# Optimization experiments

Hardware: AMD Instinct MI355X
Metric: run time of the kernel (lower is better)

Reference implementation:

```python
import jax, jax.numpy as jnp
import numpy as np

TEMPERATURE = 0.07
MSE_WEIGHT = 0.5
SUPCON_WEIGHT = 1.0
EPS = 1e-12  # F.normalize default eps

P_POS = 4000
P_NEG = 4000
NVOX = 32768
FEAT = 128


def setup_inputs() -> dict:
    key = jax.random.key(0)
    k1, k2, k3, k4, k5 = jax.random.split(key, 5)
    Zs = jax.random.normal(k1, (1, FEAT, NVOX), dtype=jnp.float32)
    pos_idx = jax.random.randint(k2, (P_POS,), 0, NVOX, dtype=jnp.int32)
    neg_idx = jax.random.randint(k3, (P_NEG,), 0, NVOX, dtype=jnp.int32)
    feature_diff = jax.random.normal(k4, (1, FEAT, 32, 32, 32), dtype=jnp.float32)
    input_diff = jax.random.normal(k5, (1, FEAT, 32, 32, 32), dtype=jnp.float32)
    return {"Zs": Zs, "pos_idx": pos_idx, "neg_idx": neg_idx,
            "feature_diff": feature_diff, "input_diff": input_diff}


def _l2_normalize_rows(x):
    # F.normalize(x, dim=1): x / max(||x||_2, eps)
    n = jnp.sqrt(jnp.sum(x * x, axis=1, keepdims=True))
    return x / jnp.maximum(n, EPS)


def _supcon_loss(Zs, pos_idx, neg_idx):
    feats = Zs[0].T                                   # [Nvox, F]
    pixels = jnp.concatenate([feats[pos_idx], feats[neg_idx]], axis=0)  # [N, F]
    n = pixels.shape[0]
    labels = jnp.concatenate([jnp.ones((P_POS,), jnp.int32),
                              jnp.zeros((P_NEG,), jnp.int32)])
    pixels = _l2_normalize_rows(pixels)
    dot = jnp.matmul(pixels, pixels.T) / TEMPERATURE  # [N, N]
    dot = _l2_normalize_rows(dot)                     # row-normalize the NxN matrix
    expm = jnp.exp(dot)
    class_mask = (labels[:, None] == labels[None, :]) & ~jnp.eye(n, dtype=bool)
    pos_term = expm * class_mask
    pos_term = jnp.where(pos_term == 0, 1.0, pos_term)
    denom = jnp.sum(expm * ~class_mask, axis=1) - jnp.diagonal(expm)  # [N]
    full_term = jnp.log(pos_term) - jnp.log(denom)[None, :]
    return -(1.0 / n) * jnp.sum(full_term)


def reference(Zs, pos_idx, neg_idx, feature_diff, input_diff):
    supcon = _supcon_loss(Zs, pos_idx, neg_idx)
    mse = jnp.mean((feature_diff - input_diff) ** 2)
    return SUPCON_WEIGHT * supcon + MSE_WEIGHT * mse
```

## Files before the change

### kernel.cpp

```cpp
#include <hip/hip_runtime.h>
#include <hip/hip_bf16.h>
#include <math.h>

typedef unsigned short u16;
typedef float  f32x4  __attribute__((ext_vector_type(4)));
typedef __bf16 bf16x8 __attribute__((ext_vector_type(8)));

#define NPOS   4000
#define LDP    136
#define TILE_CH 2176
#define MSE_N  4194304
#define GATHER_B 2000
#define MSE_B    512

__device__ __forceinline__ void load_lds16(const void* g, void* l) {
  __builtin_amdgcn_global_load_lds(
      (const __attribute__((address_space(1))) unsigned int*)g,
      (__attribute__((address_space(3))) unsigned int*)l, 16, 0, 0);
}

__device__ __forceinline__ float bf2f(u16 h) {
  unsigned u = ((unsigned)h) << 16;
  return __builtin_bit_cast(float, u);
}

struct Args {
  const float* Zs; const int* pos; const int* neg;
  const float4* fd; const float4* idf;
  u16* Pc; u16* Prow; float* G; float* S;
  float* qpos; float* qneg; float* sdpos; float* sdneg;
  float* msepart; float* out;
};

__global__ __launch_bounds__(256) void prep_k(Args a) {
  int blk = blockIdx.x, tid = threadIdx.x;
  int wave = tid >> 6, lane = tid & 63;
  if (blk < GATHER_B) {
    int row = blk * 4 + wave;
    int col = (row < NPOS) ? row : (4096 + row - NPOS);
    int v   = (row < NPOS) ? a.pos[row] : a.neg[row - NPOS];
    const float* zc = a.Zs + v;
    float x0 = zc[(size_t)lane << 15];
    float x1 = zc[(size_t)(lane + 64) << 15];
    float s = x0 * x0 + x1 * x1;
    #pragma unroll
    for (int o = 1; o < 64; o <<= 1) s += __shfl_xor(s, o, 64);
    float inv = 1.0f / fmaxf(sqrtf(s), 1e-12f);
    __hip_bfloat16 h0 = __float2bfloat16(x0 * inv);
    __hip_bfloat16 h1 = __float2bfloat16(x1 * inv);
    u16 b0 = *(u16*)&h0, b1 = *(u16*)&h1;
    a.Prow[(size_t)col * LDP + lane]      = b0;
    a.Prow[(size_t)col * LDP + lane + 64] = b1;
    size_t cbase = (size_t)(col >> 7) * (128 * LDP) + (col & 127);
    a.Pc[cbase + (size_t)lane * LDP]        = b0;
    a.Pc[cbase + (size_t)(lane + 64) * LDP] = b1;
  } else if (blk < GATHER_B + MSE_B) {
    int b = blk - GATHER_B;
    float ms = 0.f;
    for (int idx = b * 256 + tid; idx < MSE_N / 4; idx += MSE_B * 256) {
      float4 u = a.fd[idx], w = a.idf[idx];
      float dx = u.x - w.x, dy = u.y - w.y, dz = u.z - w.z, dv = u.w - w.w;
      ms += dx * dx + dy * dy + dz * dz + dv * dv;
    }
    #pragma unroll
    for (int o = 1; o < 64; o <<= 1) ms += __shfl_xor(ms, o, 64);
    __shared__ float red[4];
    if (lane == 0) red[wave] = ms;
    __syncthreads();
    if (tid == 0) a.msepart[b] = red[0] + red[1] + red[2] + red[3];
  } else {
    int ch = (blk == GATHER_B + MSE_B) ? 31 : 63;
    for (int e = tid; e < 128 * 96; e += 256) {
      int f = e / 96, c = 32 + e % 96;
      a.Pc[(size_t)ch * (128 * LDP) + (size_t)f * LDP + c] = 0;
    }
  }
}

__global__ __launch_bounds__(256) void syrk_k(Args a) {
  __shared__ __align__(16) u16 T0[128 * LDP];
  int blk = blockIdx.x, tid = threadIdx.x;
  int wave = tid >> 6, lane = tid & 63;
  int wm = (wave >> 1) << 6, wn = (wave & 1) << 6;
  int r = lane & 15, q = lane >> 4;
  int sf = tid >> 1, sh = tid & 1;
  float ssum = 0.f;
  f32x4 acc[4][4];
  #pragma unroll
  for (int x = 0; x < 4; ++x)
    #pragma unroll
    for (int y = 0; y < 4; ++y) {
      acc[x][y][0] = 0.f; acc[x][y][1] = 0.f; acc[x][y][2] = 0.f; acc[x][y][3] = 0.f;
    }
  for (int it = 0; it < 4; ++it) {
    const u16* g = a.Pc + (size_t)(blk * 4 + it) * (128 * LDP);
    #pragma unroll
    for (int k = 0; k < 9; ++k) {
      int cc = k * 256 + tid;
      if (cc < TILE_CH) load_lds16(g + cc * 8, &T0[cc * 8]);
    }
    __syncthreads();
    #pragma unroll
    for (int kk = 0; kk < 4; ++kk) {
      int k0 = kk * 32 + q * 8;
      bf16x8 af[4], bfr[4];
      #pragma unroll
      for (int t = 0; t < 4; ++t) {
        af[t]  = *(const bf16x8*)&T0[(wm + t * 16 + r) * LDP + k0];
        bfr[t] = *(const bf16x8*)&T0[(wn + t * 16 + r) * LDP + k0];
      }
      #pragma unroll
      for (int mt = 0; mt < 4; ++mt)
        #pragma unroll
        for (int nt = 0; nt < 4; ++nt)
          acc[mt][nt] = __builtin_amdgcn_mfma_f32_16x16x32_bf16(
              af[mt], bfr[nt], acc[mt][nt], 0, 0, 0);
    }
    {
      const u16* base = &T0[sf * LDP + sh * 64];
      #pragma unroll
      for (int vb = 0; vb < 8; ++vb) {
        bf16x8 v = *(const bf16x8*)&base[vb * 8];
        #pragma unroll
        for (int j = 0; j < 8; ++j) ssum += (float)v[j];
      }
    }
    __syncthreads();
  }
  float* Gf = a.G + (size_t)(blk >> 3) * 16384;
  #pragma unroll
  for (int mt = 0; mt < 4; ++mt)
    #pragma unroll
    for (int nt = 0; nt < 4; ++nt)
      #pragma unroll
      for (int reg = 0; reg < 4; ++reg) {
        int ar = wm + mt * 16 + q * 4 + reg;
        int bc = wn + nt * 16 + r;
        atomicAdd(&Gf[ar * 128 + bc], acc[mt][nt][reg]);
      }
  ssum += __shfl_xor(ssum, 1, 64);
  if (sh == 0) atomicAdd(&a.S[(blk >> 3) * 128 + sf], ssum);
}

__global__ __launch_bounds__(256) void quad_k(Args a) {
  __shared__ __align__(16) u16 T0[128 * LDP];
  __shared__ __align__(16) u16 T1[128 * LDP];
  __shared__ float Sl[256];
  __shared__ float qld[2][128];
  int cb = blockIdx.x & 63, set = blockIdx.x >> 6, tid = threadIdx.x;
  Sl[tid] = a.S[tid];
  const u16* gP = a.Prow + (size_t)cb * (128 * LDP);
  #pragma unroll
  for (int k = 0; k < 9; ++k) {
    int cc = k * 256 + tid;
    if (cc < TILE_CH) load_lds16(gP + cc * 8, &T1[cc * 8]);
  }
  {
    int f = tid >> 1, half = (tid & 1) * 64;
    const float4* gsrc = (const float4*)(a.G + (size_t)set * 16384 + f * 128 + half);
    #pragma unroll
    for (int j16 = 0; j16 < 16; ++j16) {
      float4 v = gsrc[j16];
      __hip_bfloat16 c0 = __float2bfloat16(v.x), c1 = __float2bfloat16(v.y);
      __hip_bfloat16 c2 = __float2bfloat16(v.z), c3 = __float2bfloat16(v.w);
      ushort4 pk = { *(u16*)&c0, *(u16*)&c1, *(u16*)&c2, *(u16*)&c3 };
      *(ushort4*)&T0[f * LDP + half + j16 * 4] = pk;
    }
  }
  __syncthreads();
  int wave = tid >> 6, lane = tid & 63;
  int wm = (wave >> 1) << 6, wn = (wave & 1) << 6;
  int r = lane & 15, q = lane >> 4;
  f32x4 acc[4][4];
  #pragma unroll
  for (int x = 0; x < 4; ++x)
    #pragma unroll
    for (int y = 0; y < 4; ++y) {
      acc[x][y][0] = 0.f; acc[x][y][1] = 0.f; acc[x][y][2] = 0.f; acc[x][y][3] = 0.f;
    }
  #pragma unroll
  for (int kk = 0; kk < 4; ++kk) {
    int k0 = kk * 32 + q * 8;
    bf16x8 af[4], bfr[4];
    #pragma unroll
    for (int t = 0; t < 4; ++t) {
      af[t]  = *(const bf16x8*)&T0[(wm + t * 16 + r) * LDP + k0];
      bfr[t] = *(const bf16x8*)&T1[(wn + t * 16 + r) * LDP + k0];
    }
    #pragma unroll
    for (int mt = 0; mt < 4; ++mt)
      #pragma unroll
      for (int nt = 0; nt < 4; ++nt)
        acc[mt][nt] = __builtin_amdgcn_mfma_f32_16x16x32_bf16(
            af[mt], bfr[nt], acc[mt][nt], 0, 0, 0);
  }
  float qv[4] = {0.f, 0.f, 0.f, 0.f};
  #pragma unroll
  for (int nt = 0; nt < 4; ++nt) {
    int il = wn + nt * 16 + r;
    #pragma unroll
    for (int mt = 0; mt < 4; ++mt) {
      const u16* pp = &T1[il * LDP + wm + mt * 16 + q * 4];
      #pragma unroll
      for (int reg = 0; reg < 4; ++reg)
        qv[nt] += acc[mt][nt][reg] * bf2f(pp[reg]);
    }
  }
  #pragma unroll
  for (int nt = 0; nt < 4; ++nt) {
    qv[nt] += __shfl_xor(qv[nt], 16, 64);
    qv[nt] += __shfl_xor(qv[nt], 32, 64);
  }
  int half = wm >> 6;
  if (q == 0) {
    #pragma unroll
    for (int nt = 0; nt < 4; ++nt) qld[half][wn + nt * 16 + r] = qv[nt];
  }
  __syncthreads();
  float* qarr = set ? a.qneg : a.qpos;
  if (tid < 128) qarr[cb * 128 + tid] = qld[0][tid] + qld[1][tid];
  if (set == 0) {
    int which = tid >> 7, sl = tid & 127;
    const float* Sv = &Sl[which * 128];
    float d = 0.f;
    #pragma unroll
    for (int fb = 0; fb < 16; ++fb) {
      const u16* pv = &T1[sl * LDP + fb * 8];
      #pragma unroll
      for (int j = 0; j < 8; ++j) d += Sv[fb * 8 + j] * bf2f(pv[j]);
    }
    (which ? a.sdneg : a.sdpos)[cb * 128 + sl] = d;
  }
}

__global__ __launch_bounds__(256) void final_k(Args a) {
  int tid = threadIdx.x;
  int wave = tid >> 6, lane = tid & 63;
  float lg = 0.f, sm = 0.f;
  for (int col = tid; col < 8192; col += 256) {
    bool isp = col < NPOS;
    bool isn = (col >= 4096) && (col < 4096 + NPOS);
    if (isp || isn) {
      float qp = a.qpos[col], qn = a.qneg[col];
      float c = 1.0f / sqrtf(qp + qn);
      float qo  = isp ? qn : qp;
      float sdo = isp ? a.sdneg[col] : a.sdpos[col];
      float sds = isp ? a.sdpos[col] : a.sdneg[col];
      float denom = 4000.0f + c * sdo + 0.5f * c * c * qo;
      lg += logf(denom);
      sm += c * (sds - 1.0f);
    }
  }
  float ms = a.msepart[tid] + a.msepart[tid + 256];
  #pragma unroll
  for (int o = 1; o < 64; o <<= 1) {
    lg += __shfl_xor(lg, o, 64);
    sm += __shfl_xor(sm, o, 64);
    ms += __shfl_xor(ms, o, 64);
  }
  __shared__ float redf[12];
  if (lane == 0) { redf[wave] = lg; redf[4 + wave] = sm; redf[8 + wave] = ms; }
  __syncthreads();
  if (tid == 0) {
    float lgs = redf[0] + redf[1] + redf[2] + redf[3];
    float sms = redf[4] + redf[5] + redf[6] + redf[7];
    float mss = redf[8] + redf[9] + redf[10] + redf[11];
    a.out[0] = lgs - sms * (1.0f / 8000.0f) + 0.5f * (mss * (1.0f / (float)MSE_N));
  }
}

extern "C" void kernel_launch(void* const* d_in, const int* in_sizes, int n_in,
                              void* d_out, int out_size, void* d_ws, size_t ws_size,
                              hipStream_t stream) {
  char* ws = (char*)d_ws;
  Args args;
  args.Zs  = (const float*)d_in[0];
  args.pos = (const int*)d_in[1];
  args.neg = (const int*)d_in[2];
  args.fd  = (const float4*)d_in[3];
  args.idf = (const float4*)d_in[4];
  args.out = (float*)d_out;

  args.Pc      = (u16*)(ws + 0);
  args.Prow    = (u16*)(ws + 2228224);
  args.G       = (float*)(ws + 4456448);
  args.S       = (float*)(ws + 4587520);
  args.qpos    = (float*)(ws + 4588544);
  args.qneg    = (float*)(ws + 4621312);
  args.sdpos   = (float*)(ws + 4654080);
  args.sdneg   = (float*)(ws + 4686848);
  args.msepart = (float*)(ws + 4719616);

  hipMemsetAsync(ws + 4456448, 0, 132096, stream);
  prep_k<<<GATHER_B + MSE_B + 2, 256, 0, stream>>>(args);
  syrk_k<<<16, 256, 0, stream>>>(args);
  quad_k<<<128, 256, 0, stream>>>(args);
  final_k<<<1, 256, 0, stream>>>(args);
}
```

Baseline: 139.4 us.

## Gather via coalesced voxel tiles in LDS and fold memset into prep kernel

Instead of each wave doing strided 128 KB-stride scalar loads for one gathered voxel, each of 256 blocks loads a 128-voxel slab of Zs coalesced into LDS, scans all pos/neg indices to find matches in its range, and normalizes those rows from LDS. This reads all of Zs (16 MB) rather than scattered elements, trading extra bandwidth for coalescing. It also replaces the hipMemsetAsync of the G/S workspace with two extra blocks in prep_k, removing one launch. Each block rescans all 8000 indices, and the 1024-entry match list assumes no slab receives more than 1024 hits.

Measured after the change: 133.5 us (median of 2 runs). 1.04x faster.

```diff
diff --git a/kernel.cpp b/kernel.cpp
--- a/kernel.cpp
+++ b/kernel.cpp
@@ -10,8 +10,9 @@
 #define LDP    136
 #define TILE_CH 2176
 #define MSE_N  4194304
-#define GATHER_B 2000
+#define GATHER_B 256
 #define MSE_B    512
+#define TLD    132
 
 __device__ __forceinline__ void load_lds16(const void* g, void* l) {
   __builtin_amdgcn_global_load_lds(
@@ -33,27 +34,54 @@
 };
 
 __global__ __launch_bounds__(256) void prep_k(Args a) {
+  __shared__ __align__(16) float tile[128 * TLD];
+  __shared__ int mlist[1024];
+  __shared__ int mcnt;
   int blk = blockIdx.x, tid = threadIdx.x;
   int wave = tid >> 6, lane = tid & 63;
   if (blk < GATHER_B) {
-    int row = blk * 4 + wave;
-    int col = (row < NPOS) ? row : (4096 + row - NPOS);
-    int v   = (row < NPOS) ? a.pos[row] : a.neg[row - NPOS];
-    const float* zc = a.Zs + v;
-    float x0 = zc[(size_t)lane << 15];
-    float x1 = zc[(size_t)(lane + 64) << 15];
-    float s = x0 * x0 + x1 * x1;
-    #pragma unroll
-    for (int o = 1; o < 64; o <<= 1) s += __shfl_xor(s, o, 64);
-    float inv = 1.0f / fmaxf(sqrtf(s), 1e-12f);
-    __hip_bfloat16 h0 = __float2bfloat16(x0 * inv);
-    __hip_bfloat16 h1 = __float2bfloat16(x1 * inv);
-    u16 b0 = *(u16*)&h0, b1 = *(u16*)&h1;
-    a.Prow[(size_t)col * LDP + lane]      = b0;
-    a.Prow[(size_t)col * LDP + lane + 64] = b1;
-    size_t cbase = (size_t)(col >> 7) * (128 * LDP) + (col & 127);
-    a.Pc[cbase + (size_t)lane * LDP]        = b0;
-    a.Pc[cbase + (size_t)(lane + 64) * LDP] = b1;
+    int v0 = blk << 7;
+    if (tid == 0) mcnt = 0;
+    __syncthreads();
+    {
+      int rq = tid >> 5;
+      int c4 = (tid & 31) << 2;
+      #pragma unroll
+      for (int p = 0; p < 16; ++p) {
+        int f = p * 8 + rq;
+        float4 v = *(const float4*)(a.Zs + ((size_t)f << 15) + v0 + c4);
+        *(float4*)&tile[f * TLD + c4] = v;
+      }
+    }
+    for (int k = 0; k < 4000; k += 256) {
+      int i = k + tid;
+      if (i < 4000) {
+        unsigned dp = (unsigned)(a.pos[i] - v0);
+        if (dp < 128u) { int m = atomicAdd(&mcnt, 1); mlist[m] = (i << 7) | dp; }
+        unsigned dn = (unsigned)(a.neg[i] - v0);
+        if (dn < 128u) { int m = atomicAdd(&mcnt, 1); mlist[m] = ((4096 + i) << 7) | dn; }
+      }
+    }
+    __syncthreads();
+    int nm = mcnt;
+    for (int m = wave; m < nm; m += 4) {
+      int e = mlist[m];
+      int col = e >> 7, lv = e & 127;
+      float x0 = tile[lane * TLD + lv];
+      float x1 = tile[(lane + 64) * TLD + lv];
+      float s = x0 * x0 + x1 * x1;
+      #pragma unroll
+      for (int o = 1; o < 64; o <<= 1) s += __shfl_xor(s, o, 64);
+      float inv = 1.0f / fmaxf(sqrtf(s), 1e-12f);
+      __hip_bfloat16 h0 = __float2bfloat16(x0 * inv);
+      __hip_bfloat16 h1 = __float2bfloat16(x1 * inv);
+      u16 b0 = *(u16*)&h0, b1 = *(u16*)&h1;
+      a.Prow[(size_t)col * LDP + lane]      = b0;
+      a.Prow[(size_t)col * LDP + lane + 64] = b1;
+      size_t cbase = (size_t)(col >> 7) * (128 * LDP) + (col & 127);
+      a.Pc[cbase + (size_t)lane * LDP]        = b0;
+      a.Pc[cbase + (size_t)(lane + 64) * LDP] = b1;
+    }
   } else if (blk < GATHER_B + MSE_B) {
     int b = blk - GATHER_B;
     float ms = 0.f;
@@ -68,12 +96,16 @@
     if (lane == 0) red[wave] = ms;
     __syncthreads();
     if (tid == 0) a.msepart[b] = red[0] + red[1] + red[2] + red[3];
-  } else {
+  } else if (blk < GATHER_B + MSE_B + 2) {
     int ch = (blk == GATHER_B + MSE_B) ? 31 : 63;
     for (int e = tid; e < 128 * 96; e += 256) {
       int f = e / 96, c = 32 + e % 96;
       a.Pc[(size_t)ch * (128 * LDP) + (size_t)f * LDP + c] = 0;
     }
+  } else {
+    int b = blk - (GATHER_B + MSE_B + 2);
+    float4 z = {0.f, 0.f, 0.f, 0.f};
+    for (int i = b * 256 + tid; i < 8256; i += 512) ((float4*)a.G)[i] = z;
   }
 }
 
@@ -291,8 +323,7 @@
   args.sdneg   = (float*)(ws + 4686848);
   args.msepart = (float*)(ws + 4719616);
 
-  hipMemsetAsync(ws + 4456448, 0, 132096, stream);
-  prep_k<<<GATHER_B + MSE_B + 2, 256, 0, stream>>>(args);
+  prep_k<<<GATHER_B + MSE_B + 4, 256, 0, stream>>>(args);
   syrk_k<<<16, 256, 0, stream>>>(args);
   quad_k<<<128, 256, 0, stream>>>(args);
   final_k<<<1, 256, 0, stream>>>(args);
```
